# Kernel optimization log

Hardware: AMD Instinct MI355X
Metric: run time of the kernel (lower is better)

## Reference

```python
import jax, jax.numpy as jnp
import numpy as np

D_MODEL = 2048
N_HEADS = 16
D_K = D_MODEL // N_HEADS
MAX_SEQ = 2048
THETA = 10000.0


def _rope(x, token_positions):
    # x: [B, H, S, d_k], token_positions: [S] int
    freqs = 1.0 / THETA ** (jnp.arange(0, D_K, 2, dtype=jnp.float32) / D_K)  # [d_k/2]
    angles = token_positions.astype(jnp.float32)[:, None] * freqs[None, :]   # [S, d_k/2]
    cos, sin = jnp.cos(angles), jnp.sin(angles)
    x_even, x_odd = x[..., 0::2], x[..., 1::2]
    out_even = x_even * cos - x_odd * sin
    out_odd = x_even * sin + x_odd * cos
    return jnp.stack([out_even, out_odd], axis=-1).reshape(x.shape)


def setup_inputs() -> dict:
    key = jax.random.key(0)
    ks = jax.random.split(key, 5)
    B, S = 2, 2048
    std = np.sqrt(2.0 / (D_MODEL + D_MODEL))
    def w(k):
        return (jax.random.truncated_normal(k, -3.0, 3.0, (D_MODEL, D_MODEL), jnp.float32) * std)
    return {
        "x": jax.random.normal(ks[0], (B, S, D_MODEL), jnp.float32),
        "wq": w(ks[1]), "wk": w(ks[2]), "wv": w(ks[3]), "wo": w(ks[4]),
        "token_positions": jnp.arange(S, dtype=jnp.int32),
    }


def reference(x, wq, wk, wv, wo, token_positions):
    B, S, _ = x.shape
    # Linear: einsum('... i, o i -> ... o')
    def proj(w):
        h = jnp.einsum('bsi,oi->bso', x, w)
        return h.reshape(B, S, N_HEADS, D_K).transpose(0, 2, 1, 3)  # [B,H,S,d_k]
    Q, K, V = proj(wq), proj(wk), proj(wv)
    Q = _rope(Q, token_positions)
    K = _rope(K, token_positions)
    scores = jnp.einsum('bhqd,bhkd->bhqk', Q, K) / jnp.sqrt(jnp.float32(D_K))
    causal = jnp.tril(jnp.ones((S, S), dtype=bool))
    scores = jnp.where(causal, scores, -jnp.inf)
    attn = jax.nn.softmax(scores, axis=-1)
    out = jnp.einsum('bhqk,bhkd->bhqd', attn, V)
    out = out.transpose(0, 2, 1, 3).reshape(B, S, D_MODEL)
    return jnp.einsum('bsi,oi->bso', out, wo)
```

## Files before the change

kernel.cpp:

```cpp
#include <hip/hip_runtime.h>
#include <stdint.h>
#include <stddef.h>

typedef unsigned short u16;
typedef unsigned int u32;
typedef __attribute__((ext_vector_type(8))) short s8v;
typedef __attribute__((ext_vector_type(4))) short s4v;
typedef __attribute__((ext_vector_type(4))) float f4v;

#define D_MODEL 2048
#define NH 16
#define DK 128

__device__ __forceinline__ float b2f(u16 u) {
    union { u32 i; float f; } v; v.i = ((u32)u) << 16; return v.f;
}
__device__ __forceinline__ u16 f2b(float f) {
    u32 u = __builtin_bit_cast(u32, f);
    u32 r = (u + 0x7fffu + ((u >> 16) & 1u)) >> 16;
    return (u16)r;
}
__device__ __forceinline__ float fexp2(float x) {
    return __builtin_amdgcn_exp2f(x);
}
__device__ __forceinline__ f4v mfma16(s8v a, s8v b, f4v c) {
    return __builtin_amdgcn_mfma_f32_16x16x32_bf16(a, b, c, 0, 0, 0);
}
__device__ __forceinline__ void gload_lds16(const void* g, void* l) {
    __builtin_amdgcn_global_load_lds(
        (const __attribute__((address_space(1))) u32*)(uintptr_t)g,
        (__attribute__((address_space(3))) u32*)(uintptr_t)l, 16, 0, 0);
}

__device__ __forceinline__ void store_out(u16* p, float v)   { *p = f2b(v); }
__device__ __forceinline__ void store_out(float* p, float v) { *p = v; }

__global__ __launch_bounds__(256) void cvt_bf16(
    const float* __restrict__ s0, const float* __restrict__ s1,
    const float* __restrict__ s2, const float* __restrict__ s3,
    const float* __restrict__ s4,
    u16* __restrict__ d0, u16* __restrict__ d1, u16* __restrict__ d2,
    u16* __restrict__ d3, u16* __restrict__ d4,
    int n0, int nw)
{
    const int seg = blockIdx.y;
    const float* s = (seg == 0) ? s0 : (seg == 1) ? s1 : (seg == 2) ? s2 : (seg == 3) ? s3 : s4;
    u16*         d = (seg == 0) ? d0 : (seg == 1) ? d1 : (seg == 2) ? d2 : (seg == 3) ? d3 : d4;
    const int    n = (seg == 0) ? n0 : nw;
    int i = (blockIdx.x * 256 + threadIdx.x) * 8;
    if (i >= n) return;
    f4v a = *(const f4v*)(s + i);
    f4v b = *(const f4v*)(s + i + 4);
    s8v o;
    o[0] = (short)f2b(a[0]); o[1] = (short)f2b(a[1]);
    o[2] = (short)f2b(a[2]); o[3] = (short)f2b(a[3]);
    o[4] = (short)f2b(b[0]); o[5] = (short)f2b(b[1]);
    o[6] = (short)f2b(b[2]); o[7] = (short)f2b(b[3]);
    *(s8v*)(d + i) = o;
}

template<typename OutT>
__global__ __launch_bounds__(512) void gemm_bt3(
    const u16* __restrict__ A,
    const u16* __restrict__ B0, const u16* __restrict__ B1, const u16* __restrict__ B2,
    OutT* __restrict__ C0, OutT* __restrict__ C1, OutT* __restrict__ C2,
    int M, int N, int K)
{
    const int z = blockIdx.z;
    const u16* Bp = (z == 0) ? B0 : (z == 1) ? B1 : B2;
    OutT*      Cp = (z == 0) ? C0 : (z == 1) ? C1 : C2;

    __shared__ short As[2 * 256 * 64];
    __shared__ short Bs[2 * 128 * 64];

    const int t    = threadIdx.x;
    const int lane = t & 63;
    const int w    = t >> 6;
    const int wr   = w >> 1;
    const int wc   = w & 1;
    const int m0   = blockIdx.x * 256;
    const int n0   = blockIdx.y * 128;

    const int srow = t >> 3;
    const int scol = (((t & 7) ^ ((t >> 3) & 7)) * 8);

    const u16* gA = A  + (size_t)(m0 + srow) * K + scol;
    const u16* gB = Bp + (size_t)(n0 + srow) * K + scol;
    char* lA = (char*)As + (size_t)w * 1024;
    char* lB = (char*)Bs + (size_t)w * 1024;
    const size_t rstep = (size_t)64 * K;

    const int fr = lane & 15;
    const int g4 = lane >> 4;
    const int xa = fr & 7;

    f4v acc[4][4];
#pragma unroll
    for (int i = 0; i < 4; i++)
#pragma unroll
        for (int j = 0; j < 4; j++) acc[i][j] = (f4v){0.f, 0.f, 0.f, 0.f};

    const int NT = K / 64;

    auto STAGE = [&](int p, int kt) {
        const u16* a = gA + (size_t)kt * 64;
        const u16* b = gB + (size_t)kt * 64;
        char* la = lA + p * 32768;
        char* lb = lB + p * 16384;
#pragma unroll
        for (int i = 0; i < 4; i++)
            gload_lds16(a + (size_t)i * rstep, la + i * 8192);
#pragma unroll
        for (int i = 0; i < 2; i++)
            gload_lds16(b + (size_t)i * rstep, lb + i * 8192);
    };

    STAGE(0, 0);
    if (NT > 1) STAGE(1, 1);

    for (int kt = 0; kt < NT; kt++) {
        const int p = kt & 1;
        if (kt < NT - 1) asm volatile("s_waitcnt vmcnt(6)" ::: "memory");
        else             asm volatile("s_waitcnt vmcnt(0)" ::: "memory");
        asm volatile("s_barrier" ::: "memory");

        const short* Ab = As + p * 16384;
        const short* Bb = Bs + p * 8192;
#pragma unroll
        for (int ks = 0; ks < 2; ks++) {
            const int sl = ((ks * 4 + g4) ^ xa) * 8;
            s8v aF[4], bF[4];
#pragma unroll
            for (int mi = 0; mi < 4; mi++)
                aF[mi] = *(const s8v*)&Ab[(wr * 64 + mi * 16 + fr) * 64 + sl];
#pragma unroll
            for (int ni = 0; ni < 4; ni++)
                bF[ni] = *(const s8v*)&Bb[(wc * 64 + ni * 16 + fr) * 64 + sl];
            __builtin_amdgcn_s_setprio(1);
#pragma unroll
            for (int mi = 0; mi < 4; mi++)
#pragma unroll
                for (int ni = 0; ni < 4; ni++)
                    acc[mi][ni] = mfma16(aF[mi], bF[ni], acc[mi][ni]);
            __builtin_amdgcn_s_setprio(0);
        }

        asm volatile("s_barrier" ::: "memory");
        if (kt + 2 < NT) STAGE(p, kt + 2);
    }

    const int rg = g4 * 4;
#pragma unroll
    for (int mi = 0; mi < 4; mi++)
#pragma unroll
        for (int ni = 0; ni < 4; ni++) {
            size_t base = (size_t)(m0 + wr * 64 + mi * 16 + rg) * N
                        + (n0 + wc * 64 + ni * 16 + fr);
#pragma unroll
            for (int r = 0; r < 4; r++)
                store_out(&Cp[base + (size_t)r * N], acc[mi][ni][r]);
        }
}

__global__ void rope_kernel(u32* __restrict__ Q, u32* __restrict__ Kb,
                            const int* __restrict__ pos, int total, int S)
{
    int idx = blockIdx.x * 256 + threadIdx.x;
    if (idx >= total) return;
    int row = idx >> 10;
    int pr  = idx & 1023;
    int i   = pr & 63;
    int s   = row % S;
    float p    = (float)pos[s];
    float freq = __expf((float)i * -0.14391156831212787f);
    float ang  = p * freq;
    float c = cosf(ang), sn = sinf(ang);

    u32 qp = Q[idx];
    float qe = b2f((u16)(qp & 0xffffu)), qo = b2f((u16)(qp >> 16));
    const float sc = 0.12751919968793342f;
    float qe2 = (qe * c - qo * sn) * sc;
    float qo2 = (qe * sn + qo * c) * sc;
    Q[idx] = (u32)f2b(qe2) | ((u32)f2b(qo2) << 16);

    u32 kp = Kb[idx];
    float ke = b2f((u16)(kp & 0xffffu)), ko = b2f((u16)(kp >> 16));
    float ke2 = ke * c - ko * sn;
    float ko2 = ke * sn + ko * c;
    Kb[idx] = (u32)f2b(ke2) | ((u32)f2b(ko2) << 16);
}

__global__ __launch_bounds__(256) void transpose_v(
    const u16* __restrict__ V, u16* __restrict__ Vt, int S)
{
    __shared__ short Tl[64 * 72];
    const int t  = threadIdx.x;
    const int s0 = blockIdx.x * 64;
    const int o0 = blockIdx.y * 64;
    const int b  = blockIdx.z;
    const int r  = t >> 3;
    const int c8 = (t & 7) * 8;
#pragma unroll
    for (int i = 0; i < 2; i++) {
        int row = r + i * 32;
        *(s8v*)&Tl[row * 72 + c8] =
            *(const s8v*)(V + ((size_t)b * S + s0 + row) * D_MODEL + o0 + c8);
    }
    __syncthreads();
#pragma unroll
    for (int i = 0; i < 2; i++) {
        int orow = r + i * 32;
        s8v v;
#pragma unroll
        for (int j = 0; j < 8; j++)
            v[j] = Tl[(c8 + j) * 72 + orow];
        *(s8v*)(Vt + ((size_t)b * D_MODEL + o0 + orow) * S + s0 + c8) = v;
    }
}

#define AKV 64
#define VP  72
#define PP  72

__global__ __launch_bounds__(256) void attn_kernel(
    const u16* __restrict__ Qg, const u16* __restrict__ Kg,
    const u16* __restrict__ Vtg, u16* __restrict__ Og, int S)
{
    __shared__ short Kbuf[2][64 * 128];
    __shared__ short Vbuf[2][128 * VP];
    __shared__ short Ps[4][32 * PP];

    const int t    = threadIdx.x;
    const int lane = t & 63;
    const int w    = t >> 6;
    const int fr   = lane & 15;
    const int g4   = lane >> 4;
    const int xfr  = (fr & 7) << 3;

    const int d_ = blockIdx.x;
    const int tt = d_ >> 3;
    const int G  = ((tt & 3) << 3) | (d_ & 7);
    const int p  = tt >> 2;
    const int h  = G & 15;
    const int b  = G >> 4;
    const int ntq = S / 128;

    const u16* Qb  = Qg + ((size_t)b * S) * D_MODEL + (size_t)h * DK;
    const u16* Kb  = Kg + ((size_t)b * S) * D_MODEL + (size_t)h * DK;
    const u16* Vtb = Vtg + ((size_t)b * D_MODEL + (size_t)h * DK) * S;
    u16*       Ob  = Og + ((size_t)b * S) * D_MODEL + (size_t)h * DK;

    const int krow = t >> 4;
    const int kc8  = (t & 15) * 8;
    const int kxor = (krow & 7) << 3;
    const int vd   = t >> 3;
    const int vk8  = (t & 7) * 8;

    for (int half = 0; half < 2; half++) {
        const int T   = half ? (ntq - 1 - p) : p;
        const int q0  = T * 128;
        const int nkv = 2 * T + 2;

        s8v qf[2][4];
#pragma unroll
        for (int s = 0; s < 2; s++)
#pragma unroll
            for (int ks = 0; ks < 4; ks++)
                qf[s][ks] = *(const s8v*)(Qb +
                    (size_t)(q0 + s * 64 + w * 16 + fr) * D_MODEL + ks * 32 + g4 * 8);

        s8v kreg[4], vreg[4];
#pragma unroll
        for (int c = 0; c < 4; c++) {
            kreg[c] = *(const s8v*)(Kb + (size_t)(krow + 16 * c) * D_MODEL + kc8);
            vreg[c] = *(const s8v*)(Vtb + (size_t)(32 * c + vd) * S + vk8);
        }
        __syncthreads();
#pragma unroll
        for (int c = 0; c < 4; c++)
            *(s8v*)&Kbuf[0][(krow + 16 * c) * 128 + (kc8 ^ kxor)] = kreg[c];
#pragma unroll
        for (int c = 0; c < 4; c++)
            *(s8v*)&Vbuf[0][(32 * c + vd) * VP + vk8] = vreg[c];
        __syncthreads();

        float m_st[2] = {-1e30f, -1e30f};
        float l_st[2] = {0.f, 0.f};
        f4v accO[2][8];
#pragma unroll
        for (int s = 0; s < 2; s++)
#pragma unroll
            for (int df = 0; df < 8; df++) accO[s][df] = (f4v){0.f, 0.f, 0.f, 0.f};

        for (int kt = 0; kt < nkv; kt++) {
            const int  kv0  = kt * AKV;
            const int  buf  = kt & 1;
            const bool last = (kt + 1 == nkv);
            const bool do0  = (kv0 < q0 + 64);

            if (!last) {
                const size_t kvn = (size_t)(kt + 1) * AKV;
#pragma unroll
                for (int c = 0; c < 4; c++) {
                    kreg[c] = *(const s8v*)(Kb + (kvn + krow + 16 * c) * D_MODEL + kc8);
                    vreg[c] = *(const s8v*)(Vtb + (size_t)(32 * c + vd) * S + kvn + vk8);
                }
            }

            f4v sacc[2][4];
#pragma unroll
            for (int s = 0; s < 2; s++)
#pragma unroll
                for (int i = 0; i < 4; i++) sacc[s][i] = (f4v){0.f, 0.f, 0.f, 0.f};
#pragma unroll
            for (int ks = 0; ks < 4; ks++) {
                s8v kfr[4];
#pragma unroll
                for (int kf = 0; kf < 4; kf++)
                    kfr[kf] = *(const s8v*)&Kbuf[buf][(kf * 16 + fr) * 128 +
                                                     ((ks * 32 + g4 * 8) ^ xfr)];
                if (do0) {
#pragma unroll
                    for (int kf = 0; kf < 4; kf++)
                        sacc[0][kf] = mfma16(kfr[kf], qf[0][ks], sacc[0][kf]);
                }
#pragma unroll
                for (int kf = 0; kf < 4; kf++)
                    sacc[1][kf] = mfma16(kfr[kf], qf[1][ks], sacc[1][kf]);
            }

#pragma unroll
            for (int s = 0; s < 2; s++) {
                if (s == 0 && !do0) continue;
                const int qg = q0 + s * 64 + w * 16 + fr;
                if (kv0 == q0 + s * 64) {
#pragma unroll
                    for (int kf = 0; kf < 4; kf++)
#pragma unroll
                        for (int r = 0; r < 4; r++)
                            if (kv0 + kf * 16 + g4 * 4 + r > qg)
                                sacc[s][kf][r] = -1e30f;
                }
                float rm = -1e30f;
#pragma unroll
                for (int kf = 0; kf < 4; kf++)
                    rm = fmaxf(rm, fmaxf(fmaxf(sacc[s][kf][0], sacc[s][kf][1]),
                                         fmaxf(sacc[s][kf][2], sacc[s][kf][3])));
                rm = fmaxf(rm, __shfl_xor(rm, 16));
                rm = fmaxf(rm, __shfl_xor(rm, 32));
                if (__any(rm > m_st[s])) {
                    float mn   = fmaxf(m_st[s], rm);
                    float corr = fexp2(m_st[s] - mn);
                    l_st[s] *= corr;
#pragma unroll
                    for (int df = 0; df < 8; df++) {
                        accO[s][df][0] *= corr; accO[s][df][1] *= corr;
                        accO[s][df][2] *= corr; accO[s][df][3] *= corr;
                    }
                    m_st[s] = mn;
                }
                float rsum = 0.f;
#pragma unroll
                for (int kf = 0; kf < 4; kf++) {
                    float p0 = fexp2(sacc[s][kf][0] - m_st[s]);
                    float p1 = fexp2(sacc[s][kf][1] - m_st[s]);
                    float p2 = fexp2(sacc[s][kf][2] - m_st[s]);
                    float p3 = fexp2(sacc[s][kf][3] - m_st[s]);
                    rsum += (p0 + p1) + (p2 + p3);
                    s4v pk;
                    pk[0] = (short)f2b(p0); pk[1] = (short)f2b(p1);
                    pk[2] = (short)f2b(p2); pk[3] = (short)f2b(p3);
                    *(s4v*)&Ps[w][(s * 16 + fr) * PP + kf * 16 + g4 * 4] = pk;
                }
                rsum += __shfl_xor(rsum, 16);
                rsum += __shfl_xor(rsum, 32);
                l_st[s] += rsum;
            }

#pragma unroll
            for (int ks = 0; ks < 2; ks++) {
                s8v pf0, pf1;
                if (do0) pf0 = *(const s8v*)&Ps[w][fr * PP + ks * 32 + g4 * 8];
                pf1 = *(const s8v*)&Ps[w][(16 + fr) * PP + ks * 32 + g4 * 8];
#pragma unroll
                for (int df = 0; df < 8; df++) {
                    s8v vf = *(const s8v*)&Vbuf[buf][(df * 16 + fr) * VP +
                                                     ks * 32 + g4 * 8];
                    if (do0) accO[0][df] = mfma16(vf, pf0, accO[0][df]);
                    accO[1][df] = mfma16(vf, pf1, accO[1][df]);
                }
            }

            if (!last) {
#pragma unroll
                for (int c = 0; c < 4; c++)
                    *(s8v*)&Kbuf[buf ^ 1][(krow + 16 * c) * 128 + (kc8 ^ kxor)] = kreg[c];
#pragma unroll
                for (int c = 0; c < 4; c++)
                    *(s8v*)&Vbuf[buf ^ 1][(32 * c + vd) * VP + vk8] = vreg[c];
            }
            __syncthreads();
        }

        short* OL = (short*)&Kbuf[0][0];
#pragma unroll
        for (int s = 0; s < 2; s++) {
            float inv = 1.f / l_st[s];
#pragma unroll
            for (int df = 0; df < 8; df++) {
                s4v ov;
                ov[0] = (short)f2b(accO[s][df][0] * inv);
                ov[1] = (short)f2b(accO[s][df][1] * inv);
                ov[2] = (short)f2b(accO[s][df][2] * inv);
                ov[3] = (short)f2b(accO[s][df][3] * inv);
                *(s4v*)&OL[(s * 64 + w * 16 + fr) * 128 + ((df * 16 + g4 * 4) ^ xfr)] = ov;
            }
        }
        __syncthreads();
#pragma unroll
        for (int i = 0; i < 8; i++) {
            int row = i * 16 + (t >> 4);
            int ch  = (t & 15) * 8;
            s8v v = *(const s8v*)&OL[row * 128 + (ch ^ ((row & 7) << 3))];
            *(s8v*)(Ob + (size_t)(q0 + row) * D_MODEL + ch) = v;
        }
    }
}

extern "C" void kernel_launch(void* const* d_in, const int* in_sizes, int n_in,
                              void* d_out, int out_size, void* d_ws, size_t ws_size,
                              hipStream_t stream)
{
    const float* x  = (const float*)d_in[0];
    const float* wq = (const float*)d_in[1];
    const float* wk = (const float*)d_in[2];
    const float* wv = (const float*)d_in[3];
    const float* wo = (const float*)d_in[4];
    const int*   tp = (const int*)d_in[5];

    const int S  = in_sizes[5];
    const int BS = in_sizes[0] / D_MODEL;
    const int Bn = BS / S;
    const int NW = D_MODEL * D_MODEL;
    const int NX = BS * D_MODEL;

    u16* Qw  = (u16*)d_ws;
    u16* Kw  = Qw + (size_t)NX;
    u16* Vw  = Kw + (size_t)NX;
    u16* Xb  = Vw + (size_t)NX;
    u16* Wqb = Xb + (size_t)NX;
    u16* Wkb = Wqb + (size_t)NW;
    u16* Wvb = Wkb + (size_t)NW;
    u16* Wob = Wvb + (size_t)NW;

    {
        dim3 g((NX / 8 + 255) / 256, 5);
        cvt_bf16<<<g, 256, 0, stream>>>(x, wq, wk, wv, wo,
                                        Xb, Wqb, Wkb, Wvb, Wob, NX, NW);
    }

    dim3 gq(BS / 256, D_MODEL / 128, 3);
    gemm_bt3<u16><<<gq, 512, 0, stream>>>(Xb, Wqb, Wkb, Wvb, Qw, Kw, Vw,
                                          BS, D_MODEL, D_MODEL);

    int total = BS * (D_MODEL / 2);
    rope_kernel<<<(total + 255) / 256, 256, 0, stream>>>((u32*)Qw, (u32*)Kw, tp, total, S);
    transpose_v<<<dim3(S / 64, D_MODEL / 64, Bn), 256, 0, stream>>>(Vw, Xb, S);

    attn_kernel<<<dim3((S / 256) * NH * Bn, 1, 1), 256, 0, stream>>>(Qw, Kw, Xb, Vw, S);

    dim3 go(BS / 256, D_MODEL / 128, 1);
    gemm_bt3<float><<<go, 512, 0, stream>>>(Vw, Wob, Wob, Wob,
                                            (float*)d_out, (float*)d_out, (float*)d_out,
                                            BS, D_MODEL, D_MODEL);
}
```

Baseline: 285.8 us.

## Triple-buffer GEMM with interleaved stage/compute phases; widen attention to 8 waves

The GEMM moves from a double-buffered loop to a three-stage LDS pipeline. Each K tile is split into four quarter-phases that interleave global-to-LDS loads with MFMA chunks, separated by barriers, to hide load latency and spread LDS reads. The attention kernel doubles its block to 512 threads so each wave owns 16 query rows instead of 32. Waves whose query range lies entirely before a KV tile skip it, giving finer causal skipping and more waves in flight. The cost is many more barriers per K tile in the GEMM, higher LDS use (three buffers), and a heavier K/V staging load per thread count ratio in attention.

```diff
diff --git a/kernel.cpp b/kernel.cpp
--- a/kernel.cpp
+++ b/kernel.cpp
@@ -34,6 +34,9 @@
 
 __device__ __forceinline__ void store_out(u16* p, float v)   { *p = f2b(v); }
 __device__ __forceinline__ void store_out(float* p, float v) { *p = v; }
+
+#define SBAR()   asm volatile("s_barrier" ::: "memory")
+#define VMCNT(n) asm volatile("s_waitcnt vmcnt(" #n ")" ::: "memory")
 
 __global__ __launch_bounds__(256) void cvt_bf16(
     const float* __restrict__ s0, const float* __restrict__ s1,
@@ -60,7 +63,7 @@
 }
 
 template<typename OutT>
-__global__ __launch_bounds__(512) void gemm_bt3(
+__global__ __launch_bounds__(512) void gemm8(
     const u16* __restrict__ A,
     const u16* __restrict__ B0, const u16* __restrict__ B1, const u16* __restrict__ B2,
     OutT* __restrict__ C0, OutT* __restrict__ C1, OutT* __restrict__ C2,
@@ -70,8 +73,8 @@
     const u16* Bp = (z == 0) ? B0 : (z == 1) ? B1 : B2;
     OutT*      Cp = (z == 0) ? C0 : (z == 1) ? C1 : C2;
 
-    __shared__ short As[2 * 256 * 64];
-    __shared__ short Bs[2 * 128 * 64];
+    __shared__ short As[3 * 256 * 64];
+    __shared__ short Bs[3 * 128 * 64];
 
     const int t    = threadIdx.x;
     const int lane = t & 63;
@@ -100,54 +103,85 @@
 #pragma unroll
         for (int j = 0; j < 4; j++) acc[i][j] = (f4v){0.f, 0.f, 0.f, 0.f};
 
+    auto stageA = [&](int p, int kt, int h) {
+        const u16* g = gA + (size_t)kt * 64;
+#pragma unroll
+        for (int j = 0; j < 2; j++)
+            gload_lds16(g + (size_t)(2 * h + j) * rstep,
+                        lA + p * 32768 + (2 * h + j) * 8192);
+    };
+    auto stageB = [&](int p, int kt) {
+        const u16* g = gB + (size_t)kt * 64;
+#pragma unroll
+        for (int j = 0; j < 2; j++)
+            gload_lds16(g + (size_t)j * rstep,
+                        lB + p * 16384 + j * 8192);
+    };
+    auto loadA = [&](int p, int mh, int ks, s8v* aF) {
+        const short* base = As + p * 16384;
+        const int sl = ((ks * 4 + g4) ^ xa) * 8;
+#pragma unroll
+        for (int j = 0; j < 2; j++)
+            aF[j] = *(const s8v*)&base[(wr * 64 + (mh * 2 + j) * 16 + fr) * 64 + sl];
+    };
+    auto loadB = [&](int p, int ks, s8v* bF) {
+        const short* base = Bs + p * 8192;
+        const int sl = ((ks * 4 + g4) ^ xa) * 8;
+#pragma unroll
+        for (int ni = 0; ni < 4; ni++)
+            bF[ni] = *(const s8v*)&base[(wc * 64 + ni * 16 + fr) * 64 + sl];
+    };
+    auto mfc = [&](int mh, s8v* aF, s8v* bF) {
+        __builtin_amdgcn_s_setprio(1);
+#pragma unroll
+        for (int j = 0; j < 2; j++)
+#pragma unroll
+            for (int ni = 0; ni < 4; ni++)
+                acc[mh * 2 + j][ni] = mfma16(aF[j], bF[ni], acc[mh * 2 + j][ni]);
+        __builtin_amdgcn_s_setprio(0);
+    };
+
     const int NT = K / 64;
-
-    auto STAGE = [&](int p, int kt) {
-        const u16* a = gA + (size_t)kt * 64;
-        const u16* b = gB + (size_t)kt * 64;
-        char* la = lA + p * 32768;
-        char* lb = lB + p * 16384;
-#pragma unroll
-        for (int i = 0; i < 4; i++)
-            gload_lds16(a + (size_t)i * rstep, la + i * 8192);
-#pragma unroll
-        for (int i = 0; i < 2; i++)
-            gload_lds16(b + (size_t)i * rstep, lb + i * 8192);
-    };
-
-    STAGE(0, 0);
-    if (NT > 1) STAGE(1, 1);
-
-    for (int kt = 0; kt < NT; kt++) {
-        const int p = kt & 1;
-        if (kt < NT - 1) asm volatile("s_waitcnt vmcnt(6)" ::: "memory");
-        else             asm volatile("s_waitcnt vmcnt(0)" ::: "memory");
-        asm volatile("s_barrier" ::: "memory");
-
-        const short* Ab = As + p * 16384;
-        const short* Bb = Bs + p * 8192;
-#pragma unroll
-        for (int ks = 0; ks < 2; ks++) {
-            const int sl = ((ks * 4 + g4) ^ xa) * 8;
-            s8v aF[4], bF[4];
-#pragma unroll
-            for (int mi = 0; mi < 4; mi++)
-                aF[mi] = *(const s8v*)&Ab[(wr * 64 + mi * 16 + fr) * 64 + sl];
-#pragma unroll
-            for (int ni = 0; ni < 4; ni++)
-                bF[ni] = *(const s8v*)&Bb[(wc * 64 + ni * 16 + fr) * 64 + sl];
-            __builtin_amdgcn_s_setprio(1);
-#pragma unroll
-            for (int mi = 0; mi < 4; mi++)
-#pragma unroll
-                for (int ni = 0; ni < 4; ni++)
-                    acc[mi][ni] = mfma16(aF[mi], bF[ni], acc[mi][ni]);
-            __builtin_amdgcn_s_setprio(0);
-        }
-
-        asm volatile("s_barrier" ::: "memory");
-        if (kt + 2 < NT) STAGE(p, kt + 2);
+    const int NI = NT / 2;
+
+    stageA(0, 0, 0); stageA(0, 0, 1); stageB(0, 0);
+    stageA(1, 1, 0); stageA(1, 1, 1); stageB(1, 1);
+    VMCNT(6);
+    SBAR();
+
+    int s0 = 0, s1 = 1, s2 = 2;
+    for (int i = 0; i < NI; i++) {
+        const int k2 = (2 * i + 2 < NT) ? 2 * i + 2 : 0;
+        const int k3 = (2 * i + 3 < NT) ? 2 * i + 3 : 1;
+        s8v aF[2], bF[4];
+
+        loadB(s0, 0, bF); loadA(s0, 0, 0, aF);
+        stageA(s2, k2, 0);
+        SBAR(); mfc(0, aF, bF); SBAR();
+        loadA(s0, 1, 0, aF);
+        stageA(s2, k2, 1);
+        SBAR(); mfc(1, aF, bF); SBAR();
+        loadB(s0, 1, bF); loadA(s0, 0, 1, aF);
+        stageB(s2, k2);
+        SBAR(); mfc(0, aF, bF); SBAR();
+        loadA(s0, 1, 1, aF);
+        VMCNT(6); SBAR(); mfc(1, aF, bF); SBAR();
+        loadB(s1, 0, bF); loadA(s1, 0, 0, aF);
+        stageA(s0, k3, 0);
+        SBAR(); mfc(0, aF, bF); SBAR();
+        loadA(s1, 1, 0, aF);
+        stageA(s0, k3, 1);
+        SBAR(); mfc(1, aF, bF); SBAR();
+        loadB(s1, 1, bF); loadA(s1, 0, 1, aF);
+        stageB(s0, k3);
+        SBAR(); mfc(0, aF, bF); SBAR();
+        loadA(s1, 1, 1, aF);
+        VMCNT(6); SBAR(); mfc(1, aF, bF); SBAR();
+
+        const int ns0 = s2, ns1 = s0, ns2 = s1;
+        s0 = ns0; s1 = ns1; s2 = ns2;
     }
+    VMCNT(0);
 
     const int rg = g4 * 4;
 #pragma unroll
@@ -222,13 +256,13 @@
 #define VP  72
 #define PP  72
 
-__global__ __launch_bounds__(256) void attn_kernel(
+__global__ __launch_bounds__(512) void attn_kernel(
     const u16* __restrict__ Qg, const u16* __restrict__ Kg,
     const u16* __restrict__ Vtg, u16* __restrict__ Og, int S)
 {
     __shared__ short Kbuf[2][64 * 128];
     __shared__ short Vbuf[2][128 * VP];
-    __shared__ short Ps[4][32 * PP];
+    __shared__ short Ps[8][16 * PP];
 
     const int t    = threadIdx.x;
     const int lane = t & 63;
@@ -256,170 +290,150 @@
     const int vd   = t >> 3;
     const int vk8  = (t & 7) * 8;
 
+    const int wq64 = (w >> 2) * 64;
+
     for (int half = 0; half < 2; half++) {
         const int T   = half ? (ntq - 1 - p) : p;
         const int q0  = T * 128;
         const int nkv = 2 * T + 2;
 
-        s8v qf[2][4];
-#pragma unroll
-        for (int s = 0; s < 2; s++)
-#pragma unroll
-            for (int ks = 0; ks < 4; ks++)
-                qf[s][ks] = *(const s8v*)(Qb +
-                    (size_t)(q0 + s * 64 + w * 16 + fr) * D_MODEL + ks * 32 + g4 * 8);
-
-        s8v kreg[4], vreg[4];
-#pragma unroll
-        for (int c = 0; c < 4; c++) {
-            kreg[c] = *(const s8v*)(Kb + (size_t)(krow + 16 * c) * D_MODEL + kc8);
-            vreg[c] = *(const s8v*)(Vtb + (size_t)(32 * c + vd) * S + vk8);
+        s8v qf[4];
+#pragma unroll
+        for (int ks = 0; ks < 4; ks++)
+            qf[ks] = *(const s8v*)(Qb +
+                (size_t)(q0 + w * 16 + fr) * D_MODEL + ks * 32 + g4 * 8);
+
+        s8v kreg[2], vreg[2];
+#pragma unroll
+        for (int c = 0; c < 2; c++) {
+            kreg[c] = *(const s8v*)(Kb + (size_t)(krow + 32 * c) * D_MODEL + kc8);
+            vreg[c] = *(const s8v*)(Vtb + (size_t)(vd + 64 * c) * S + vk8);
         }
         __syncthreads();
 #pragma unroll
-        for (int c = 0; c < 4; c++)
-            *(s8v*)&Kbuf[0][(krow + 16 * c) * 128 + (kc8 ^ kxor)] = kreg[c];
-#pragma unroll
-        for (int c = 0; c < 4; c++)
-            *(s8v*)&Vbuf[0][(32 * c + vd) * VP + vk8] = vreg[c];
+        for (int c = 0; c < 2; c++)
+            *(s8v*)&Kbuf[0][(krow + 32 * c) * 128 + (kc8 ^ kxor)] = kreg[c];
+#pragma unroll
+        for (int c = 0; c < 2; c++)
+            *(s8v*)&Vbuf[0][(vd + 64 * c) * VP + vk8] = vreg[c];
         __syncthreads();
 
-        float m_st[2] = {-1e30f, -1e30f};
-        float l_st[2] = {0.f, 0.f};
-        f4v accO[2][8];
-#pragma unroll
-        for (int s = 0; s < 2; s++)
-#pragma unroll
-            for (int df = 0; df < 8; df++) accO[s][df] = (f4v){0.f, 0.f, 0.f, 0.f};
+        float m_st = -1e30f, l_st = 0.f;
+        f4v accO[8];
+#pragma unroll
+        for (int df = 0; df < 8; df++) accO[df] = (f4v){0.f, 0.f, 0.f, 0.f};
+        const int qg = q0 + w * 16 + fr;
 
         for (int kt = 0; kt < nkv; kt++) {
             const int  kv0  = kt * AKV;
             const int  buf  = kt & 1;
             const bool last = (kt + 1 == nkv);
-            const bool do0  = (kv0 < q0 + 64);
+            const bool act  = (kv0 <= q0 + wq64);
 
             if (!last) {
                 const size_t kvn = (size_t)(kt + 1) * AKV;
 #pragma unroll
-                for (int c = 0; c < 4; c++) {
-                    kreg[c] = *(const s8v*)(Kb + (kvn + krow + 16 * c) * D_MODEL + kc8);
-                    vreg[c] = *(const s8v*)(Vtb + (size_t)(32 * c + vd) * S + kvn + vk8);
+                for (int c = 0; c < 2; c++) {
+                    kreg[c] = *(const s8v*)(Kb + (kvn + krow + 32 * c) * D_MODEL + kc8);
+                    vreg[c] = *(const s8v*)(Vtb + (size_t)(vd + 64 * c) * S + kvn + vk8);
                 }
             }
 
-            f4v sacc[2][4];
-#pragma unroll
-            for (int s = 0; s < 2; s++)
-#pragma unroll
-                for (int i = 0; i < 4; i++) sacc[s][i] = (f4v){0.f, 0.f, 0.f, 0.f};
-#pragma unroll
-            for (int ks = 0; ks < 4; ks++) {
-                s8v kfr[4];
-#pragma unroll
-                for (int kf = 0; kf < 4; kf++)
-                    kfr[kf] = *(const s8v*)&Kbuf[buf][(kf * 16 + fr) * 128 +
-                                                     ((ks * 32 + g4 * 8) ^ xfr)];
-                if (do0) {
-#pragma unroll
-                    for (int kf = 0; kf < 4; kf++)
-                        sacc[0][kf] = mfma16(kfr[kf], qf[0][ks], sacc[0][kf]);
-                }
-#pragma unroll
-                for (int kf = 0; kf < 4; kf++)
-                    sacc[1][kf] = mfma16(kfr[kf], qf[1][ks], sacc[1][kf]);
-            }
-
-#pragma unroll
-            for (int s = 0; s < 2; s++) {
-                if (s == 0 && !do0) continue;
-                const int qg = q0 + s * 64 + w * 16 + fr;
-                if (kv0 == q0 + s * 64) {
+            if (act) {
+                f4v sacc[4];
+#pragma unroll
+                for (int i = 0; i < 4; i++) sacc[i] = (f4v){0.f, 0.f, 0.f, 0.f};
+#pragma unroll
+                for (int ks = 0; ks < 4; ks++) {
+#pragma unroll
+                    for (int kf = 0; kf < 4; kf++) {
+                        s8v kfr = *(const s8v*)&Kbuf[buf][(kf * 16 + fr) * 128 +
+                                                         ((ks * 32 + g4 * 8) ^ xfr)];
+                        sacc[kf] = mfma16(kfr, qf[ks], sacc[kf]);
+                    }
+                }
+
+                if (kv0 == q0 + wq64) {
 #pragma unroll
                     for (int kf = 0; kf < 4; kf++)
 #pragma unroll
                         for (int r = 0; r < 4; r++)
                             if (kv0 + kf * 16 + g4 * 4 + r > qg)
-                                sacc[s][kf][r] = -1e30f;
+                                sacc[kf][r] = -1e30f;
                 }
                 float rm = -1e30f;
 #pragma unroll
                 for (int kf = 0; kf < 4; kf++)
-                    rm = fmaxf(rm, fmaxf(fmaxf(sacc[s][kf][0], sacc[s][kf][1]),
-                                         fmaxf(sacc[s][kf][2], sacc[s][kf][3])));
+                    rm = fmaxf(rm, fmaxf(fmaxf(sacc[kf][0], sacc[kf][1]),
+                                         fmaxf(sacc[kf][2], sacc[kf][3])));
                 rm = fmaxf(rm, __shfl_xor(rm, 16));
                 rm = fmaxf(rm, __shfl_xor(rm, 32));
-                if (__any(rm > m_st[s])) {
-                    float mn   = fmaxf(m_st[s], rm);
-                    float corr = fexp2(m_st[s] - mn);
-                    l_st[s] *= corr;
+                if (__any(rm > m_st)) {
+                    float mn   = fmaxf(m_st, rm);
+                    float corr = fexp2(m_st - mn);
+                    l_st *= corr;
 #pragma unroll
                     for (int df = 0; df < 8; df++) {
-                        accO[s][df][0] *= corr; accO[s][df][1] *= corr;
-                        accO[s][df][2] *= corr; accO[s][df][3] *= corr;
+                        accO[df][0] *= corr; accO[df][1] *= corr;
+                        accO[df][2] *= corr; accO[df][3] *= corr;
                     }
-                    m_st[s] = mn;
+                    m_st = mn;
                 }
                 float rsum = 0.f;
 #pragma unroll
                 for (int kf = 0; kf < 4; kf++) {
-                    float p0 = fexp2(sacc[s][kf][0] - m_st[s]);
-                    float p1 = fexp2(sacc[s][kf][1] - m_st[s]);
-                    float p2 = fexp2(sacc[s][kf][2] - m_st[s]);
-                    float p3 = fexp2(sacc[s][kf][3] - m_st[s]);
+                    float p0 = fexp2(sacc[kf][0] - m_st);
+                    float p1 = fexp2(sacc[kf][1] - m_st);
+                    float p2 = fexp2(sacc[kf][2] - m_st);
+                    float p3 = fexp2(sacc[kf][3] - m_st);
                     rsum += (p0 + p1) + (p2 + p3);
                     s4v pk;
                     pk[0] = (short)f2b(p0); pk[1] = (short)f2b(p1);
                     pk[2] = (short)f2b(p2); pk[3] = (short)f2b(p3);
-                    *(s4v*)&Ps[w][(s * 16 + fr) * PP + kf * 16 + g4 * 4] = pk;
+                    *(s4v*)&Ps[w][fr * PP + kf * 16 + g4 * 4] = pk;
                 }
                 rsum += __shfl_xor(rsum, 16);
                 rsum += __shfl_xor(rsum, 32);
-                l_st[s] += rsum;
+                l_st += rsum;
+
+#pragma unroll
+                for (int ks = 0; ks < 2; ks++) {
+                    s8v pf = *(const s8v*)&Ps[w][fr * PP + ks * 32 + g4 * 8];
+#pragma unroll
+                    for (int df = 0; df < 8; df++) {
+                        s8v vf = *(const s8v*)&Vbuf[buf][(df * 16 + fr) * VP +
+                                                         ks * 32 + g4 * 8];
+                        accO[df] = mfma16(vf, pf, accO[df]);
+                    }
+                }
             }
 
-#pragma unroll
-            for (int ks = 0; ks < 2; ks++) {
-                s8v pf0, pf1;
-                if (do0) pf0 = *(const s8v*)&Ps[w][fr * PP + ks * 32 + g4 * 8];
-                pf1 = *(const s8v*)&Ps[w][(16 + fr) * PP + ks * 32 + g4 * 8];
-#pragma unroll
-                for (int df = 0; df < 8; df++) {
-                    s8v vf = *(const s8v*)&Vbuf[buf][(df * 16 + fr) * VP +
-                                                     ks * 32 + g4 * 8];
-                    if (do0) accO[0][df] = mfma16(vf, pf0, accO[0][df]);
-                    accO[1][df] = mfma16(vf, pf1, accO[1][df]);
-                }
-            }
-
             if (!last) {
 #pragma unroll
-                for (int c = 0; c < 4; c++)
-                    *(s8v*)&Kbuf[buf ^ 1][(krow + 16 * c) * 128 + (kc8 ^ kxor)] = kreg[c];
-#pragma unroll
-                for (int c = 0; c < 4; c++)
-                    *(s8v*)&Vbuf[buf ^ 1][(32 * c + vd) * VP + vk8] = vreg[c];
+                for (int c = 0; c < 2; c++)
+                    *(s8v*)&Kbuf[buf ^ 1][(krow + 32 * c) * 128 + (kc8 ^ kxor)] = kreg[c];
+#pragma unroll
+                for (int c = 0; c < 2; c++)
+                    *(s8v*)&Vbuf[buf ^ 1][(vd + 64 * c) * VP + vk8] = vreg[c];
             }
             __syncthreads();
         }
 
+        float inv = 1.f / l_st;
         short* OL = (short*)&Kbuf[0][0];
 #pragma unroll
-        for (int s = 0; s < 2; s++) {
-            float inv = 1.f / l_st[s];
-#pragma unroll
-            for (int df = 0; df < 8; df++) {
-                s4v ov;
-                ov[0] = (short)f2b(accO[s][df][0] * inv);
-                ov[1] = (short)f2b(accO[s][df][1] * inv);
-                ov[2] = (short)f2b(accO[s][df][2] * inv);
-                ov[3] = (short)f2b(accO[s][df][3] * inv);
-                *(s4v*)&OL[(s * 64 + w * 16 + fr) * 128 + ((df * 16 + g4 * 4) ^ xfr)] = ov;
-            }
+        for (int df = 0; df < 8; df++) {
+            s4v ov;
+            ov[0] = (short)f2b(accO[df][0] * inv);
+            ov[1] = (short)f2b(accO[df][1] * inv);
+            ov[2] = (short)f2b(accO[df][2] * inv);
+            ov[3] = (short)f2b(accO[df][3] * inv);
+            *(s4v*)&OL[(w * 16 + fr) * 128 + ((df * 16 + g4 * 4) ^ xfr)] = ov;
         }
         __syncthreads();
 #pragma unroll
-        for (int i = 0; i < 8; i++) {
-            int row = i * 16 + (t >> 4);
+        for (int i = 0; i < 4; i++) {
+            int row = i * 32 + (t >> 4);
             int ch  = (t & 15) * 8;
             s8v v = *(const s8v*)&OL[row * 128 + (ch ^ ((row & 7) << 3))];
             *(s8v*)(Ob + (size_t)(q0 + row) * D_MODEL + ch) = v;
@@ -460,17 +474,17 @@
     }
 
     dim3 gq(BS / 256, D_MODEL / 128, 3);
-    gemm_bt3<u16><<<gq, 512, 0, stream>>>(Xb, Wqb, Wkb, Wvb, Qw, Kw, Vw,
-                                          BS, D_MODEL, D_MODEL);
+    gemm8<u16><<<gq, 512, 0, stream>>>(Xb, Wqb, Wkb, Wvb, Qw, Kw, Vw,
+                                       BS, D_MODEL, D_MODEL);
 
     int total = BS * (D_MODEL / 2);
     rope_kernel<<<(total + 255) / 256, 256, 0, stream>>>((u32*)Qw, (u32*)Kw, tp, total, S);
     transpose_v<<<dim3(S / 64, D_MODEL / 64, Bn), 256, 0, stream>>>(Vw, Xb, S);
 
-    attn_kernel<<<dim3((S / 256) * NH * Bn, 1, 1), 256, 0, stream>>>(Qw, Kw, Xb, Vw, S);
+    attn_kernel<<<dim3((S / 256) * NH * Bn, 1, 1), 512, 0, stream>>>(Qw, Kw, Xb, Vw, S);
 
     dim3 go(BS / 256, D_MODEL / 128, 1);
-    gemm_bt3<float><<<go, 512, 0, stream>>>(Vw, Wob, Wob, Wob,
-                                            (float*)d_out, (float*)d_out, (float*)d_out,
-                                            BS, D_MODEL, D_MODEL);
-}
+    gemm8<float><<<go, 512, 0, stream>>>(Vw, Wob, Wob, Wob,
+                                         (float*)d_out, (float*)d_out, (float*)d_out,
+                                         BS, D_MODEL, D_MODEL);
+}
```

Measured after the change: 250.5 us. 12.4% less time.
